# Performance work log

Measured on AMD Instinct MI355X. Metric: run time of the kernel, lower is better.

## Reference

```python
import jax, jax.numpy as jnp
import numpy as np

NUM_SLOTS = 8
PATCHES_PER_SLOT = 8  # num_select // num_slots, capped by N
TEMPERATURE = 0.1
NEG_INF = -10000.0


def _l2norm(x, eps=1e-6):
    # matches F.normalize: x / max(||x||, eps)
    n = jnp.sqrt(jnp.sum(x * x, axis=-1, keepdims=True))
    return x / jnp.maximum(n, eps)


def setup_inputs() -> dict:
    key = jax.random.key(0)
    k1, k2 = jax.random.split(key)
    local_feats = jax.random.normal(k1, (64, 1024, 768), dtype=jnp.float32)
    slots = jax.random.normal(k2, (1, NUM_SLOTS, 768), dtype=jnp.float32)
    return {"local_feats": local_feats, "slots": slots}


def reference(local_feats, slots):
    B, N, D = local_feats.shape
    K = slots.shape[1]
    slots_b = jnp.broadcast_to(slots, (B, K, D))

    x = local_feats.astype(jnp.float32)
    x_norm = _l2norm(x)
    s_norm = _l2norm(slots_b.astype(jnp.float32))

    # (B, K, N) cosine logits
    attn_logits = jnp.einsum('bkd,bnd->bkn', s_norm, x_norm)

    pps = min(PATCHES_PER_SLOT, N)
    topk_val, _ = jax.lax.top_k(attn_logits, pps)
    threshold = topk_val[:, :, -1:]  # (B, K, 1)

    mask_hard = (attn_logits >= threshold).astype(jnp.float32)
    mask_soft = jax.nn.sigmoid(attn_logits / TEMPERATURE)
    # straight-through estimator
    mask = jax.lax.stop_gradient(mask_hard - mask_soft) + mask_soft

    masked_logits = attn_logits * mask + NEG_INF * (1.0 - mask)
    attn = jax.nn.softmax(masked_logits, axis=-1)

    # img-space mask: max over slots -> (B, N, 1)
    img_space_mask = jnp.max(mask, axis=1)[..., None]

    # orthogonality loss on attention gram matrix
    gram = jnp.einsum('bkn,bjn->bkj', attn, attn)
    I = jnp.eye(K, dtype=jnp.float32)
    ortho_loss = jnp.mean(jnp.abs(gram - I[None, :, :]))

    # module returns the (unupdated) expanded slots, the ortho loss, and the mask
    return slots_b, ortho_loss, img_space_mask
```

## Files before the change

kernel.cpp:

```cpp
#include <hip/hip_runtime.h>
#include <math.h>

#define BB 64
#define NN 1024
#define DD 768
#define KK 8

#define WS_SNORM   0
#define WS_LOGITS  6144
#define WS_PART    (6144 + 524288)


__global__ void k_broadcast(const float* __restrict__ slots, float* __restrict__ out) {
    const int b = blockIdx.x / 24;
    const int r = blockIdx.x % 24;
    const int idx = r * 256 + threadIdx.x;
    out[b * (KK * DD) + idx] = slots[idx];
}

__global__ void k_snorm(const float* __restrict__ slots, float* __restrict__ snorm) {
    const int k = blockIdx.x;
    const int t = threadIdx.x;
    const int lane = t & 63, wave = t >> 6;
    __shared__ float wsum[4];
    float s = 0.f;
    for (int j = t; j < DD; j += 256) {
        float v = slots[k * DD + j];
        s += v * v;
    }
#pragma unroll
    for (int off = 1; off < 64; off <<= 1) s += __shfl_xor(s, off, 64);
    if (lane == 0) wsum[wave] = s;
    __syncthreads();
    const float tot = wsum[0] + wsum[1] + wsum[2] + wsum[3];
    const float rn = 1.0f / fmaxf(sqrtf(tot), 1e-6f);
    for (int j = t; j < DD; j += 256) snorm[k * DD + j] = slots[k * DD + j] * rn;
}

__launch_bounds__(256, 2)
__global__ void k_logits(const float* __restrict__ x, const float* __restrict__ snorm,
                         float* __restrict__ logits) {
    const int b     = blockIdx.x >> 4;
    const int chunk = blockIdx.x & 15;
    const int wave  = threadIdx.x >> 6;
    const int lane  = threadIdx.x & 63;

    float4 sreg[KK][3];
#pragma unroll
    for (int k = 0; k < KK; ++k)
#pragma unroll
        for (int j = 0; j < 3; ++j)
            sreg[k][j] = *reinterpret_cast<const float4*>(snorm + k * DD + j * 256 + lane * 4);

    const int n_base = chunk * 64 + wave * 16;

    const float4* xp = reinterpret_cast<const float4*>(x + (long)(b * NN + n_base) * DD);
    float4 c0 = xp[lane], c1 = xp[64 + lane], c2 = xp[128 + lane];

    for (int i = 0; i < 16; ++i) {
        const int n = n_base + i;
        float4 p0, p1, p2;
        if (i < 15) {
            const float4* xq = reinterpret_cast<const float4*>(x + (long)(b * NN + n + 1) * DD);
            p0 = xq[lane]; p1 = xq[64 + lane]; p2 = xq[128 + lane];
        }

        float acc[KK + 1];
#pragma unroll
        for (int q = 0; q <= KK; ++q) acc[q] = 0.f;

#pragma unroll
        for (int k = 0; k < KK; ++k) {
            acc[k] = fmaf(c0.x, sreg[k][0].x, acc[k]);
            acc[k] = fmaf(c0.y, sreg[k][0].y, acc[k]);
            acc[k] = fmaf(c0.z, sreg[k][0].z, acc[k]);
            acc[k] = fmaf(c0.w, sreg[k][0].w, acc[k]);
            acc[k] = fmaf(c1.x, sreg[k][1].x, acc[k]);
            acc[k] = fmaf(c1.y, sreg[k][1].y, acc[k]);
            acc[k] = fmaf(c1.z, sreg[k][1].z, acc[k]);
            acc[k] = fmaf(c1.w, sreg[k][1].w, acc[k]);
            acc[k] = fmaf(c2.x, sreg[k][2].x, acc[k]);
            acc[k] = fmaf(c2.y, sreg[k][2].y, acc[k]);
            acc[k] = fmaf(c2.z, sreg[k][2].z, acc[k]);
            acc[k] = fmaf(c2.w, sreg[k][2].w, acc[k]);
        }
        acc[KK] = fmaf(c0.x, c0.x, acc[KK]); acc[KK] = fmaf(c0.y, c0.y, acc[KK]);
        acc[KK] = fmaf(c0.z, c0.z, acc[KK]); acc[KK] = fmaf(c0.w, c0.w, acc[KK]);
        acc[KK] = fmaf(c1.x, c1.x, acc[KK]); acc[KK] = fmaf(c1.y, c1.y, acc[KK]);
        acc[KK] = fmaf(c1.z, c1.z, acc[KK]); acc[KK] = fmaf(c1.w, c1.w, acc[KK]);
        acc[KK] = fmaf(c2.x, c2.x, acc[KK]); acc[KK] = fmaf(c2.y, c2.y, acc[KK]);
        acc[KK] = fmaf(c2.z, c2.z, acc[KK]); acc[KK] = fmaf(c2.w, c2.w, acc[KK]);

#pragma unroll
        for (int off = 1; off < 8; off <<= 1)
#pragma unroll
            for (int q = 0; q <= KK; ++q) acc[q] += __shfl_xor(acc[q], off, 64);

        float v = acc[0];
#pragma unroll
        for (int q = 1; q < KK; ++q) v = ((lane & 7) == q) ? acc[q] : v;
        float u = acc[KK];

#pragma unroll
        for (int off = 8; off < 64; off <<= 1) {
            v += __shfl_xor(v, off, 64);
            u += __shfl_xor(u, off, 64);
        }

        const float rn = 1.0f / fmaxf(sqrtf(u), 1e-6f);
        if (lane < KK) logits[(((b << 3) + lane) << 10) + n] = v * rn;

        c0 = p0; c1 = p1; c2 = p2;
    }
}

__launch_bounds__(256)
__global__ void k_select(const float* __restrict__ logits, float* __restrict__ out_mask,
                         float* __restrict__ partials) {
    const int b = blockIdx.x;
    __shared__ float lds[KK][1032];
    __shared__ float thr[KK], rmax[KK], rsum[KK];
    __shared__ float gpart[4][64];
    const int t = threadIdx.x, lane = t & 63, wave = t >> 6;

    for (int f = t; f < KK * NN; f += 256) lds[f >> 10][f & 1023] = logits[b * (KK * NN) + f];
    __syncthreads();

#pragma unroll
    for (int r = 0; r < 2; ++r) {
        const int k = wave + r * 4;
        float v[16];
#pragma unroll
        for (int i = 0; i < 16; ++i) v[i] = lds[k][i * 64 + lane];
        float th = 0.f, mx = -1e30f;
        for (int e = 0; e < 8; ++e) {
            float lv = -1e30f; int li = 0;
#pragma unroll
            for (int i = 0; i < 16; ++i) {
                if (v[i] > lv) { lv = v[i]; li = i * 64 + lane; }
            }
#pragma unroll
            for (int off = 1; off < 64; off <<= 1) {
                const float ov = __shfl_xor(lv, off, 64);
                const int   oi = __shfl_xor(li, off, 64);
                if (ov > lv || (ov == lv && oi < li)) { lv = ov; li = oi; }
            }
            if (e == 0) mx = lv;
            th = lv;
#pragma unroll
            for (int i = 0; i < 16; ++i)
                if (i * 64 + lane == li) v[i] = -1e30f;
        }
        if (lane == 0) { thr[k] = th; rmax[k] = mx; }
    }
    __syncthreads();

    for (int n = t; n < NN; n += 256) {
        float m = 0.f;
#pragma unroll
        for (int k = 0; k < KK; ++k) m = fmaxf(m, (lds[k][n] >= thr[k]) ? 1.f : 0.f);
        out_mask[b * NN + n] = m;
    }
    __syncthreads();

#pragma unroll
    for (int r = 0; r < 2; ++r) {
        const int k = wave + r * 4;
        const float th = thr[k], mx = rmax[k];
        float s = 0.f;
#pragma unroll
        for (int i = 0; i < 16; ++i) {
            const int n = i * 64 + lane;
            const float lg = lds[k][n];
            const float p = (lg >= th) ? __expf(lg - mx) : 0.f;
            lds[k][n] = p;
            s += p;
        }
#pragma unroll
        for (int off = 1; off < 64; off <<= 1) s += __shfl_xor(s, off, 64);
        if (lane == 0) rsum[k] = s;
    }
    __syncthreads();

    {
        const int k = lane >> 3, j = lane & 7;
        float s = 0.f;
#pragma unroll 8
        for (int i = 0; i < 256; ++i) {
            const int n = (wave << 8) + i;
            s += lds[k][n] * lds[j][n];
        }
        gpart[wave][lane] = s;
    }
    __syncthreads();
    if (wave == 0) {
        const int k = lane >> 3, j = lane & 7;
        float g = gpart[0][lane] + gpart[1][lane] + gpart[2][lane] + gpart[3][lane];
        g *= (1.0f / rsum[k]) * (1.0f / rsum[j]);
        float d = fabsf(g - ((k == j) ? 1.f : 0.f));
#pragma unroll
        for (int off = 1; off < 64; off <<= 1) d += __shfl_xor(d, off, 64);
        if (lane == 0) partials[b] = d;
    }
}

__global__ void k_final(const float* __restrict__ partials, float* __restrict__ out_loss) {
    const int lane = threadIdx.x;
    float v = partials[lane];
#pragma unroll
    for (int off = 1; off < 64; off <<= 1) v += __shfl_xor(v, off, 64);
    if (lane == 0) out_loss[0] = v * (1.0f / 4096.0f);
}

extern "C" void kernel_launch(void* const* d_in, const int* in_sizes, int n_in,
                              void* d_out, int out_size, void* d_ws, size_t ws_size,
                              hipStream_t stream) {
    const float* x     = (const float*)d_in[0];
    const float* slots = (const float*)d_in[1];
    float* out = (float*)d_out;
    float* ws  = (float*)d_ws;

    float* snorm    = ws + WS_SNORM;
    float* logits   = ws + WS_LOGITS;
    float* partials = ws + WS_PART;

    float* out_slots = out;
    float* out_loss  = out + 393216;
    float* out_mask  = out + 393217;

    k_broadcast<<<dim3(BB * 24), dim3(256), 0, stream>>>(slots, out_slots);
    k_snorm    <<<dim3(KK),      dim3(256), 0, stream>>>(slots, snorm);
    k_logits   <<<dim3(BB * 16), dim3(256), 0, stream>>>(x, snorm, logits);
    k_select   <<<dim3(BB),      dim3(256), 0, stream>>>(logits, out_mask, partials);
    k_final    <<<dim3(1),       dim3(64),  0, stream>>>(partials, out_loss);
}
```

Measured before the change: 307.0 us.

## Use transpose-reduce butterfly with DPP in logits; widen select and broadcast kernels

The per-row cross-lane reduction in the logits kernel now halves the data at each shuffle step, so each lane ends up owning one slot's partial sum. The last three steps use DPP adds instead of full 9-value butterfly shuffles at every step. This cuts the number of cross-lane operations per patch, which dominate the compute-light dot products. The selection kernel moves to 512 threads so each wave handles one slot, and the broadcast kernel stores float4s. The launch-bounds occupancy hint on the logits kernel is also dropped, which may change register allocation.

```diff
diff --git a/kernel.cpp b/kernel.cpp
--- a/kernel.cpp
+++ b/kernel.cpp
@@ -11,11 +11,19 @@
 #define WS_PART    (6144 + 524288)
 
 
+template <int CTRL>
+__device__ __forceinline__ float dpp_add(float x) {
+    const int xi = __float_as_int(x);
+    const int yi = __builtin_amdgcn_update_dpp(0, xi, CTRL, 0xF, 0xF, true);
+    return x + __int_as_float(yi);
+}
+
 __global__ void k_broadcast(const float* __restrict__ slots, float* __restrict__ out) {
-    const int b = blockIdx.x / 24;
-    const int r = blockIdx.x % 24;
+    const int b   = blockIdx.x / 6;
+    const int r   = blockIdx.x % 6;
     const int idx = r * 256 + threadIdx.x;
-    out[b * (KK * DD) + idx] = slots[idx];
+    reinterpret_cast<float4*>(out)[b * 1536 + idx] =
+        reinterpret_cast<const float4*>(slots)[idx];
 }
 
 __global__ void k_snorm(const float* __restrict__ slots, float* __restrict__ snorm) {
@@ -37,13 +45,14 @@
     for (int j = t; j < DD; j += 256) snorm[k * DD + j] = slots[k * DD + j] * rn;
 }
 
-__launch_bounds__(256, 2)
+__launch_bounds__(256)
 __global__ void k_logits(const float* __restrict__ x, const float* __restrict__ snorm,
                          float* __restrict__ logits) {
     const int b     = blockIdx.x >> 4;
     const int chunk = blockIdx.x & 15;
     const int wave  = threadIdx.x >> 6;
     const int lane  = threadIdx.x & 63;
+    const int b2 = (lane >> 2) & 1, b4 = (lane >> 4) & 1, b5 = (lane >> 5) & 1;
 
     float4 sreg[KK][3];
 #pragma unroll
@@ -54,20 +63,10 @@
 
     const int n_base = chunk * 64 + wave * 16;
 
-    const float4* xp = reinterpret_cast<const float4*>(x + (long)(b * NN + n_base) * DD);
-    float4 c0 = xp[lane], c1 = xp[64 + lane], c2 = xp[128 + lane];
-
-    for (int i = 0; i < 16; ++i) {
-        const int n = n_base + i;
-        float4 p0, p1, p2;
-        if (i < 15) {
-            const float4* xq = reinterpret_cast<const float4*>(x + (long)(b * NN + n + 1) * DD);
-            p0 = xq[lane]; p1 = xq[64 + lane]; p2 = xq[128 + lane];
-        }
-
-        float acc[KK + 1];
-#pragma unroll
-        for (int q = 0; q <= KK; ++q) acc[q] = 0.f;
+    auto compute_one = [&](int n, float4 c0, float4 c1, float4 c2) {
+        float acc[KK];
+#pragma unroll
+        for (int q = 0; q < KK; ++q) acc[q] = 0.f;
 
 #pragma unroll
         for (int k = 0; k < KK; ++k) {
@@ -84,51 +83,70 @@
             acc[k] = fmaf(c2.z, sreg[k][2].z, acc[k]);
             acc[k] = fmaf(c2.w, sreg[k][2].w, acc[k]);
         }
-        acc[KK] = fmaf(c0.x, c0.x, acc[KK]); acc[KK] = fmaf(c0.y, c0.y, acc[KK]);
-        acc[KK] = fmaf(c0.z, c0.z, acc[KK]); acc[KK] = fmaf(c0.w, c0.w, acc[KK]);
-        acc[KK] = fmaf(c1.x, c1.x, acc[KK]); acc[KK] = fmaf(c1.y, c1.y, acc[KK]);
-        acc[KK] = fmaf(c1.z, c1.z, acc[KK]); acc[KK] = fmaf(c1.w, c1.w, acc[KK]);
-        acc[KK] = fmaf(c2.x, c2.x, acc[KK]); acc[KK] = fmaf(c2.y, c2.y, acc[KK]);
-        acc[KK] = fmaf(c2.z, c2.z, acc[KK]); acc[KK] = fmaf(c2.w, c2.w, acc[KK]);
-
-#pragma unroll
-        for (int off = 1; off < 8; off <<= 1)
-#pragma unroll
-            for (int q = 0; q <= KK; ++q) acc[q] += __shfl_xor(acc[q], off, 64);
-
-        float v = acc[0];
-#pragma unroll
-        for (int q = 1; q < KK; ++q) v = ((lane & 7) == q) ? acc[q] : v;
-        float u = acc[KK];
-
-#pragma unroll
-        for (int off = 8; off < 64; off <<= 1) {
-            v += __shfl_xor(v, off, 64);
-            u += __shfl_xor(u, off, 64);
-        }
+        float u = 0.f;
+        u = fmaf(c0.x, c0.x, u); u = fmaf(c0.y, c0.y, u);
+        u = fmaf(c0.z, c0.z, u); u = fmaf(c0.w, c0.w, u);
+        u = fmaf(c1.x, c1.x, u); u = fmaf(c1.y, c1.y, u);
+        u = fmaf(c1.z, c1.z, u); u = fmaf(c1.w, c1.w, u);
+        u = fmaf(c2.x, c2.x, u); u = fmaf(c2.y, c2.y, u);
+        u = fmaf(c2.z, c2.z, u); u = fmaf(c2.w, c2.w, u);
+
+        float w[4];
+#pragma unroll
+        for (int j = 0; j < 4; ++j) {
+            const float send = b2 ? acc[j] : acc[j + 4];
+            const float keep = b2 ? acc[j + 4] : acc[j];
+            w[j] = keep + __shfl_xor(send, 4, 64);
+        }
+        u += __shfl_xor(u, 4, 64);
+
+        const float s0 = b4 ? w[0] : w[2];
+        const float s1 = b4 ? w[1] : w[3];
+        const float y0 = (b4 ? w[2] : w[0]) + __shfl_xor(s0, 16, 64);
+        const float y1 = (b4 ? w[3] : w[1]) + __shfl_xor(s1, 16, 64);
+        u += __shfl_xor(u, 16, 64);
+
+        const float sz = b5 ? y0 : y1;
+        float z = (b5 ? y1 : y0) + __shfl_xor(sz, 32, 64);
+        u += __shfl_xor(u, 32, 64);
+
+        z = dpp_add<0xB1>(z);   u = dpp_add<0xB1>(u);
+        z = dpp_add<0x4E>(z);   u = dpp_add<0x4E>(u);
+        z = dpp_add<0x128>(z);  u = dpp_add<0x128>(u);
 
         const float rn = 1.0f / fmaxf(sqrtf(u), 1e-6f);
-        if (lane < KK) logits[(((b << 3) + lane) << 10) + n] = v * rn;
-
+        if ((lane & 11) == 0) {
+            const int k = 4 * b2 + 2 * b4 + b5;
+            logits[(((b << 3) + k) << 10) + n] = z * rn;
+        }
+    };
+
+    const float4* xrow = reinterpret_cast<const float4*>(x + (long)(b * NN + n_base) * DD);
+    float4 c0 = xrow[lane], c1 = xrow[64 + lane], c2 = xrow[128 + lane];
+
+    for (int i = 0; i < 15; ++i) {
+        const float4* xq = xrow + (i + 1) * (DD / 4);
+        float4 p0 = xq[lane], p1 = xq[64 + lane], p2 = xq[128 + lane];
+        compute_one(n_base + i, c0, c1, c2);
         c0 = p0; c1 = p1; c2 = p2;
     }
-}
-
-__launch_bounds__(256)
+    compute_one(n_base + 15, c0, c1, c2);
+}
+
+__launch_bounds__(512)
 __global__ void k_select(const float* __restrict__ logits, float* __restrict__ out_mask,
                          float* __restrict__ partials) {
     const int b = blockIdx.x;
     __shared__ float lds[KK][1032];
     __shared__ float thr[KK], rmax[KK], rsum[KK];
-    __shared__ float gpart[4][64];
+    __shared__ float gpart[8][64];
     const int t = threadIdx.x, lane = t & 63, wave = t >> 6;
 
-    for (int f = t; f < KK * NN; f += 256) lds[f >> 10][f & 1023] = logits[b * (KK * NN) + f];
-    __syncthreads();
-
-#pragma unroll
-    for (int r = 0; r < 2; ++r) {
-        const int k = wave + r * 4;
+    for (int f = t; f < KK * NN; f += 512) lds[f >> 10][f & 1023] = logits[b * (KK * NN) + f];
+    __syncthreads();
+
+    {
+        const int k = wave;
         float v[16];
 #pragma unroll
         for (int i = 0; i < 16; ++i) v[i] = lds[k][i * 64 + lane];
@@ -155,7 +173,7 @@
     }
     __syncthreads();
 
-    for (int n = t; n < NN; n += 256) {
+    for (int n = t; n < NN; n += 512) {
         float m = 0.f;
 #pragma unroll
         for (int k = 0; k < KK; ++k) m = fmaxf(m, (lds[k][n] >= thr[k]) ? 1.f : 0.f);
@@ -163,9 +181,8 @@
     }
     __syncthreads();
 
-#pragma unroll
-    for (int r = 0; r < 2; ++r) {
-        const int k = wave + r * 4;
+    {
+        const int k = wave;
         const float th = thr[k], mx = rmax[k];
         float s = 0.f;
 #pragma unroll
@@ -186,8 +203,8 @@
         const int k = lane >> 3, j = lane & 7;
         float s = 0.f;
 #pragma unroll 8
-        for (int i = 0; i < 256; ++i) {
-            const int n = (wave << 8) + i;
+        for (int i = 0; i < 128; ++i) {
+            const int n = (wave << 7) + i;
             s += lds[k][n] * lds[j][n];
         }
         gpart[wave][lane] = s;
@@ -195,7 +212,9 @@
     __syncthreads();
     if (wave == 0) {
         const int k = lane >> 3, j = lane & 7;
-        float g = gpart[0][lane] + gpart[1][lane] + gpart[2][lane] + gpart[3][lane];
+        float g = 0.f;
+#pragma unroll
+        for (int w = 0; w < 8; ++w) g += gpart[w][lane];
         g *= (1.0f / rsum[k]) * (1.0f / rsum[j]);
         float d = fabsf(g - ((k == j) ? 1.f : 0.f));
 #pragma unroll
@@ -228,9 +247,9 @@
     float* out_loss  = out + 393216;
     float* out_mask  = out + 393217;
 
-    k_broadcast<<<dim3(BB * 24), dim3(256), 0, stream>>>(slots, out_slots);
+    k_broadcast<<<dim3(384),     dim3(256), 0, stream>>>(slots, out_slots);
     k_snorm    <<<dim3(KK),      dim3(256), 0, stream>>>(slots, snorm);
     k_logits   <<<dim3(BB * 16), dim3(256), 0, stream>>>(x, snorm, logits);
-    k_select   <<<dim3(BB),      dim3(256), 0, stream>>>(logits, out_mask, partials);
+    k_select   <<<dim3(BB),      dim3(512), 0, stream>>>(logits, out_mask, partials);
     k_final    <<<dim3(1),       dim3(64),  0, stream>>>(partials, out_loss);
 }
```

Result: faster. 297.9 us (-3.0%).
